# Optimization experiments

Hardware: AMD Instinct MI355X
Metric: run time of the kernel (lower is better)

## Reference

```python
import jax, jax.numpy as jnp
import numpy as np

H = 2048
EPS = 1e-12

def setup_inputs() -> dict:
    key = jax.random.key(0)
    ks = jax.random.split(key, 12)
    B, S = 2, 4096
    scale = 1.0 / np.sqrt(H)
    inp = {
        "hidden_states": jax.random.normal(ks[0], (B, S, H), dtype=jnp.float32),
        "token_type_ids": jax.random.randint(ks[1], (B, S), 0, 2, dtype=jnp.int32),
        "ln_gamma": jnp.ones((H,), jnp.float32),
        "ln_beta": jnp.zeros((H,), jnp.float32),
        "tw1": jax.random.uniform(ks[2], (H, H), jnp.float32, -scale, scale),
        "tb1": jnp.zeros((H,), jnp.float32),
        "tw2": jax.random.uniform(ks[3], (H, H), jnp.float32, -scale, scale),
        "tb2": jnp.zeros((H,), jnp.float32),
        "iw1": jax.random.uniform(ks[4], (H, H), jnp.float32, -scale, scale),
        "ib1": jnp.zeros((H,), jnp.float32),
        "iw2": jax.random.uniform(ks[5], (H, H), jnp.float32, -scale, scale),
        "ib2": jnp.zeros((H,), jnp.float32),
    }
    return inp

def _layernorm(x, g, b):
    mu = jnp.mean(x, axis=-1, keepdims=True)
    var = jnp.mean(jnp.square(x - mu), axis=-1, keepdims=True)
    return (x - mu) * jax.lax.rsqrt(var + EPS) * g + b

def _mlp(x, w1, b1, w2, b2):
    # Linear -> exact GELU -> Linear (torch nn.GELU default is erf-based)
    h = jax.nn.gelu(jnp.einsum('bsh,hk->bsk', x, w1) + b1, approximate=False)
    return jnp.einsum('bsk,kh->bsh', h, w2) + b2

def reference(hidden_states, token_type_ids, ln_gamma, ln_beta,
              tw1, tb1, tw2, tb2, iw1, ib1, iw2, ib2):
    xn = _layernorm(hidden_states, ln_gamma, ln_beta)
    text_mask = (token_type_ids == 0)[..., None]   # [B,S,1]
    image_mask = (token_type_ids == 1)[..., None]
    text_out = _mlp(xn, tw1, tb1, tw2, tb2) * text_mask
    image_out = _mlp(xn, iw1, ib1, iw2, ib2) * image_mask
    # dropout is identity in inference / p=0
    return hidden_states + text_out + image_out
```

## Files before the change

### kernel.cpp

```cpp
#include <hip/hip_runtime.h>
#include <hip/hip_bf16.h>


#define H_DIM 2048
#define FULLROWS 8192
#define TAILROWS 512

typedef __attribute__((ext_vector_type(8))) short s16x8;
typedef __attribute__((ext_vector_type(4))) float f32x4;
typedef __attribute__((ext_vector_type(4))) int   i32x4;

typedef __attribute__((address_space(1))) const unsigned int gu32;
typedef __attribute__((address_space(3))) unsigned int lu32;
typedef __attribute__((address_space(3))) short lds_s;

__device__ __forceinline__ void load_lds16(const void* g, void* l) {
  __builtin_amdgcn_global_load_lds((gu32*)g, (lu32*)l, 16, 0, 0);
}

__device__ __forceinline__ s16x8 asbf(i32x4 v) {
  union { i32x4 i; s16x8 s; } u; u.i = v; return u.s;
}

__global__ __launch_bounds__(256) void partition_kernel(
    const int* __restrict__ tt, int T, int* __restrict__ ctrl,
    int* __restrict__ pos, int* __restrict__ rowid) {
  __shared__ int psum[256];
  const int tid = threadIdx.x;
  const int npt = T >> 8;
  const int base = tid * npt;
  int cnt = 0;
  for (int i = 0; i < npt; ++i) cnt += (tt[base + i] == 0);
  psum[tid] = cnt;
  __syncthreads();
  for (int off = 1; off < 256; off <<= 1) {
    int v = psum[tid];
    int add = (tid >= off) ? psum[tid - off] : 0;
    __syncthreads();
    psum[tid] = v + add;
    __syncthreads();
  }
  const int Mt = psum[255];
  const int Mt_pad = (Mt + 255) & ~255;
  int tpos = psum[tid] - cnt;
  int ipos = base - tpos;
  for (int i = 0; i < npt; ++i) {
    const int tok = base + i;
    int p;
    if (tt[tok] == 0) p = tpos++;
    else              p = Mt_pad + ipos++;
    pos[tok] = p;
    rowid[p] = tok;
  }
  const int Mi = T - Mt;
  const int Mi_pad = (Mi + 255) & ~255;
  for (int g = Mt + tid; g < Mt_pad; g += 256) rowid[g] = -1;
  for (int g = Mt_pad + Mi + tid; g < Mt_pad + Mi_pad; g += 256) rowid[g] = -1;
  for (int g = Mt_pad + Mi_pad + tid; g < FULLROWS + TAILROWS; g += 256)
    rowid[g] = -1;
  if (tid == 0) {
    ctrl[0] = Mt; ctrl[1] = Mt_pad; ctrl[2] = Mi; ctrl[3] = Mi_pad;
    ctrl[4] = Mt_pad + Mi_pad;
  }
}

__global__ __launch_bounds__(256) void pad_zero_kernel(
    const int* __restrict__ ctrl, __hip_bfloat16* __restrict__ XG) {
  const int Mt = ctrl[0], Mt_pad = ctrl[1], Mi = ctrl[2];
  const int n1 = Mt_pad - Mt;
  const int start2 = Mt_pad + Mi;
  const int b = blockIdx.x;
  int row;
  if (b < n1) row = Mt + b;
  else {
    const int b2 = b - n1;
    if (start2 + b2 >= FULLROWS + TAILROWS) return;
    row = start2 + b2;
  }
  const int4 z = {0, 0, 0, 0};
  *(int4*)(XG + (size_t)row * H_DIM + threadIdx.x * 8) = z;
}

__global__ __launch_bounds__(256) void transpose_to_bf16(
    const float* __restrict__ W, __hip_bfloat16* __restrict__ WT) {
  __shared__ float tile[32][33];
  const int bx = blockIdx.x, by = blockIdx.y;
  const int tid = threadIdx.x;
  const int r = tid >> 3, c4 = (tid & 7) * 4;
  const float4 v = *(const float4*)(W + (size_t)(by * 32 + r) * H_DIM + bx * 32 + c4);
  tile[r][c4 + 0] = v.x; tile[r][c4 + 1] = v.y;
  tile[r][c4 + 2] = v.z; tile[r][c4 + 3] = v.w;
  __syncthreads();
  union { ushort u[4]; ushort4 v4; } pk;
#pragma unroll
  for (int j = 0; j < 4; ++j) {
    __hip_bfloat16 h = __float2bfloat16(tile[c4 + j][r]);
    pk.u[j] = *(const ushort*)&h;
  }
  *(ushort4*)(WT + (size_t)(bx * 32 + r) * H_DIM + by * 32 + c4) = pk.v4;
}

__global__ __launch_bounds__(256) void ln_scatter_kernel(
    const float* __restrict__ X, const float* __restrict__ gamma,
    const float* __restrict__ beta, const int* __restrict__ pos,
    __hip_bfloat16* __restrict__ XG) {
  const int t = blockIdx.x, tid = threadIdx.x;
  const float* row = X + (size_t)t * H_DIM;
  float x[8];
  {
    float4 v0 = *(const float4*)(row + tid * 8);
    float4 v1 = *(const float4*)(row + tid * 8 + 4);
    x[0] = v0.x; x[1] = v0.y; x[2] = v0.z; x[3] = v0.w;
    x[4] = v1.x; x[5] = v1.y; x[6] = v1.z; x[7] = v1.w;
  }
  float s = 0.f, q = 0.f;
#pragma unroll
  for (int j = 0; j < 8; ++j) { s += x[j]; q += x[j] * x[j]; }
#pragma unroll
  for (int off = 32; off > 0; off >>= 1) {
    s += __shfl_down(s, off);
    q += __shfl_down(q, off);
  }
  __shared__ float ls[4], lq[4];
  if ((tid & 63) == 0) { ls[tid >> 6] = s; lq[tid >> 6] = q; }
  __syncthreads();
  const float S = ls[0] + ls[1] + ls[2] + ls[3];
  const float Q = lq[0] + lq[1] + lq[2] + lq[3];
  const float mu = S * (1.0f / H_DIM);
  const float var = Q * (1.0f / H_DIM) - mu * mu;
  const float rstd = rsqrtf(var + 1e-12f);
  const int p = pos[t];
  float4 g0 = *(const float4*)(gamma + tid * 8);
  float4 g1 = *(const float4*)(gamma + tid * 8 + 4);
  float4 b0 = *(const float4*)(beta + tid * 8);
  float4 b1 = *(const float4*)(beta + tid * 8 + 4);
  float g[8] = {g0.x, g0.y, g0.z, g0.w, g1.x, g1.y, g1.z, g1.w};
  float b[8] = {b0.x, b0.y, b0.z, b0.w, b1.x, b1.y, b1.z, b1.w};
  union { ushort u[8]; int4 v; } pk;
#pragma unroll
  for (int j = 0; j < 8; ++j) {
    float y = (x[j] - mu) * rstd * g[j] + b[j];
    __hip_bfloat16 h = __float2bfloat16(y);
    pk.u[j] = *(const ushort*)&h;
  }
  *(int4*)(XG + (size_t)p * H_DIM + tid * 8) = pk.v;
}

#define DSRD(dst, addr, OFF) \
  asm volatile("ds_read_b128 %0, %1 offset:" OFF : "=v"(dst) : "v"(addr))
#define PBAR asm volatile("s_barrier" ::: "memory")
#define SB0  __builtin_amdgcn_sched_barrier(0)
#define LGKM0 do { \
  asm volatile("s_waitcnt lgkmcnt(0)" ::: "memory"); SB0; } while (0)
#define VM0 asm volatile("s_waitcnt vmcnt(0)" ::: "memory")

__device__ __forceinline__ float gelu_exact(float z) {
  return 0.5f * z * (1.0f + erff(z * 0.70710678118654752f));
}

template <int EPI>
__global__ __launch_bounds__(512, 2) void gemmk(
    const __hip_bfloat16* __restrict__ A,
    const __hip_bfloat16* __restrict__ WTt, const __hip_bfloat16* __restrict__ WTi,
    const float* __restrict__ bt, const float* __restrict__ bi,
    const int* __restrict__ ctrl, const int* __restrict__ rowid,
    __hip_bfloat16* __restrict__ Hout,
    const float* __restrict__ resid, float* __restrict__ Out,
    float* __restrict__ pp) {
  constexpr int K = H_DIM;
  const int Mt_pad = ctrl[1];

  __shared__ __align__(16) char smem[131072];
  const unsigned sBase = (unsigned)(uintptr_t)(lds_s*)smem;

  const int tid = threadIdx.x;
  const int w = tid >> 6, l = tid & 63;
  const int bid = blockIdx.x;

  const int srow8 = l >> 3;
  const int sg = (l & 7) ^ srow8;
  const int r16 = l & 15;
  const int r4base = (l >> 4) * 4;
  const int hl = (l & 15) >> 1;
  const int gr = (((l & 1) << 2) | (l >> 4)) ^ hl;

  if (bid < 256) {
    constexpr int NT = K / 64;
    const int m0 = (bid >> 3) * 256;
    const int n0 = (bid & 7) * 256;
    const bool is_text = (m0 < Mt_pad);
    const short* Ag = (const short*)A;
    const short* Bg = (const short*)(is_text ? WTt : WTi);
    const float* bias = is_text ? bt : bi;

    const int wm = w >> 2, wn = w & 3;
    const int scol8 = sg * 8;

    auto stageA = [&](int bI, int h, int kk) {
#pragma unroll
      for (int c = 0; c < 2; ++c) {
        const short* src = Ag + (size_t)(m0 + h * 128 + c * 64 + w * 8 + srow8) * K + kk + scol8;
        load_lds16(src, smem + bI * 32768 + h * 16384 + (c * 4096 + w * 512) * 2);
      }
    };
    auto stageB = [&](int bI, int h, int kk) {
#pragma unroll
      for (int c = 0; c < 2; ++c) {
        const short* src = Bg + (size_t)(n0 + h * 128 + c * 64 + w * 8 + srow8) * K + kk + scol8;
        load_lds16(src, smem + 65536 + bI * 32768 + h * 16384 + (c * 4096 + w * 512) * 2);
      }
    };

    int off2[2];
#pragma unroll
    for (int ks = 0; ks < 2; ++ks)
      off2[ks] = r16 * 64 + (((ks * 4 + (l >> 4)) ^ (l & 7)) * 8);

    unsigned ardA[2][2], ardB[2][2];
#pragma unroll
    for (int bI = 0; bI < 2; ++bI)
#pragma unroll
      for (int ks = 0; ks < 2; ++ks) {
        ardA[bI][ks] = sBase + bI * 32768u + (unsigned)(wm * 16384 + off2[ks] * 2);
        ardB[bI][ks] = sBase + 65536u + bI * 32768u +
                       (unsigned)((wn >> 1) * 16384 + ((wn & 1) * 4096 + off2[ks]) * 2);
      }

    i32x4 a[4][2], b[4][2];
    f32x4 acc[8][4];
    const f32x4 zero = {0.f, 0.f, 0.f, 0.f};
#pragma unroll
    for (int i = 0; i < 8; ++i)
#pragma unroll
      for (int j = 0; j < 4; ++j) acc[i][j] = zero;

    auto mfmaQ = [&](int fmBase, int fnBase) {
#pragma unroll
      for (int fm = 0; fm < 4; ++fm)
#pragma unroll
        for (int fn = 0; fn < 2; ++fn)
#pragma unroll
          for (int ks = 0; ks < 2; ++ks)
            acc[fmBase + fm][fnBase + fn] = __builtin_amdgcn_mfma_f32_16x16x32_bf16(
                asbf(a[fm][ks]), asbf(b[fnBase + fn][ks]),
                acc[fmBase + fm][fnBase + fn], 0, 0, 0);
    };

#define TILE(C) do {                                                          \
    DSRD(a[0][0], ardA[C][0], "0");     DSRD(a[0][1], ardA[C][1], "0");       \
    DSRD(a[1][0], ardA[C][0], "2048");  DSRD(a[1][1], ardA[C][1], "2048");    \
    DSRD(a[2][0], ardA[C][0], "4096");  DSRD(a[2][1], ardA[C][1], "4096");    \
    DSRD(a[3][0], ardA[C][0], "6144");  DSRD(a[3][1], ardA[C][1], "6144");    \
    DSRD(b[0][0], ardB[C][0], "0");     DSRD(b[0][1], ardB[C][1], "0");       \
    DSRD(b[1][0], ardB[C][0], "2048");  DSRD(b[1][1], ardB[C][1], "2048");    \
    stageA(C ^ 1, 0, _kA);                                                    \
    PBAR; LGKM0;                                                              \
    __builtin_amdgcn_s_setprio(1); mfmaQ(0, 0); __builtin_amdgcn_s_setprio(0);\
    SB0; PBAR;                                                                \
    DSRD(b[2][0], ardB[C][0], "4096");  DSRD(b[2][1], ardB[C][1], "4096");    \
    DSRD(b[3][0], ardB[C][0], "6144");  DSRD(b[3][1], ardB[C][1], "6144");    \
    stageA(C ^ 1, 1, _kA);                                                    \
    PBAR; LGKM0;                                                              \
    __builtin_amdgcn_s_setprio(1); mfmaQ(0, 2); __builtin_amdgcn_s_setprio(0);\
    SB0; PBAR;                                                                \
    DSRD(a[0][0], ardA[C][0], "8192");  DSRD(a[0][1], ardA[C][1], "8192");    \
    DSRD(a[1][0], ardA[C][0], "10240"); DSRD(a[1][1], ardA[C][1], "10240");   \
    DSRD(a[2][0], ardA[C][0], "12288"); DSRD(a[2][1], ardA[C][1], "12288");   \
    DSRD(a[3][0], ardA[C][0], "14336"); DSRD(a[3][1], ardA[C][1], "14336");   \
    stageB(C, 0, _kB);                                                        \
    PBAR; LGKM0;                                                              \
    __builtin_amdgcn_s_setprio(1); mfmaQ(4, 2); __builtin_amdgcn_s_setprio(0);\
    SB0; PBAR;                                                                \
    stageB(C, 1, _kB);                                                        \
    asm volatile("s_waitcnt vmcnt(4)" ::: "memory");                          \
    PBAR; SB0;                                                                \
    __builtin_amdgcn_s_setprio(1); mfmaQ(4, 0); __builtin_amdgcn_s_setprio(0);\
    SB0; PBAR;                                                                \
  } while (0)

    stageA(0, 0, 0); stageA(0, 1, 0);
    stageB(0, 0, 0); stageB(0, 1, 0);
    stageB(1, 0, 64); stageB(1, 1, 64);
    asm volatile("s_waitcnt vmcnt(4)" ::: "memory");
    PBAR;

    int _kA, _kB;
    for (int t = 0; t < NT; t += 2) {
      _kA = (t + 1 < NT ? t + 1 : NT - 1) * 64;
      _kB = (t + 2 < NT ? t + 2 : NT - 1) * 64;
      TILE(0);
      _kA = (t + 2 < NT ? t + 2 : NT - 1) * 64;
      _kB = (t + 3 < NT ? t + 3 : NT - 1) * 64;
      TILE(1);
    }
#undef TILE
    asm volatile("s_waitcnt vmcnt(0) lgkmcnt(0)" ::: "memory");

    float bb[4];
#pragma unroll
    for (int fn = 0; fn < 4; ++fn) bb[fn] = bias[n0 + wn * 64 + fn * 16 + r16];
    if (EPI == 0) {
#pragma unroll
      for (int fm = 0; fm < 8; ++fm) {
        const int grow = m0 + wm * 128 + fm * 16 + r4base;
#pragma unroll
        for (int fn = 0; fn < 4; ++fn) {
          const int gcol = n0 + wn * 64 + fn * 16 + r16;
          f32x4 v = acc[fm][fn];
#pragma unroll
          for (int i = 0; i < 4; ++i)
            Hout[(size_t)(grow + i) * K + gcol] = __float2bfloat16(gelu_exact(v[i] + bb[fn]));
        }
      }
    } else {
#pragma unroll
      for (int fm = 0; fm < 8; ++fm) {
        const int grow = m0 + wm * 128 + fm * 16 + r4base;
        int rid[4];
#pragma unroll
        for (int i = 0; i < 4; ++i) rid[i] = rowid[grow + i];
#pragma unroll
        for (int fn = 0; fn < 4; ++fn) {
          const int gcol = n0 + wn * 64 + fn * 16 + r16;
          f32x4 v = acc[fm][fn];
#pragma unroll
          for (int i = 0; i < 4; ++i) {
            if (rid[i] >= 0) {
              const size_t o = (size_t)rid[i] * K + gcol;
              Out[o] = resid[o] + v[i] + bb[fn];
            }
          }
        }
      }
    }
  } else {
    const int tb = bid - 256;
    const int kp = tb & 3;
    const int n0 = ((tb >> 2) & 7) * 256;
    const int m0 = FULLROWS + (tb >> 5) * 128;
    const int kk0 = kp * 512;
    const bool is_text = (m0 < Mt_pad);
    const short* Ag = (const short*)A;
    const short* Bg = (const short*)(is_text ? WTt : WTi);

    const int wm = w >> 2, wn = w & 3;
    const int sRowAdj = sg >> 2;
    const int sKAdj = (sg & 3) * 8;

    auto stageA = [&](int bI, int kk) {
      const int mr = w * 8 + srow8;
      const short* src = Ag + (size_t)(m0 + mr * 2 + sRowAdj) * K + kk + sKAdj;
      load_lds16(src, smem + bI * 8192 + w * 1024);
    };
    auto stageB = [&](int bI, int c2, int kk) {
      const int mr = c2 * 64 + w * 8 + srow8;
      const short* src = Bg + (size_t)(n0 + mr * 2 + sRowAdj) * K + kk + sKAdj;
      load_lds16(src, smem + 16384 + bI * 16384 + c2 * 8192 + w * 1024);
    };

    unsigned ardA[2], ardB[2];
#pragma unroll
    for (int bI = 0; bI < 2; ++bI) {
      ardA[bI] = sBase + bI * 8192u + (unsigned)(wm * 4096 + hl * 128 + gr * 16);
      ardB[bI] = sBase + 16384u + bI * 16384u + (unsigned)(wn * 4096 + hl * 128 + gr * 16);
    }

    i32x4 a[4], b[4];
    f32x4 acc[4][4];
    const f32x4 zero = {0.f, 0.f, 0.f, 0.f};
#pragma unroll
    for (int i = 0; i < 4; ++i)
#pragma unroll
      for (int j = 0; j < 4; ++j) acc[i][j] = zero;

#define RD_TILE(C) do {                                                   \
    DSRD(a[0], ardA[C], "0");    DSRD(a[1], ardA[C], "1024");             \
    DSRD(a[2], ardA[C], "2048"); DSRD(a[3], ardA[C], "3072");             \
    DSRD(b[0], ardB[C], "0");    DSRD(b[1], ardB[C], "1024");             \
    DSRD(b[2], ardB[C], "2048"); DSRD(b[3], ardB[C], "3072");             \
  } while (0)

    stageA(0, kk0);
    stageB(0, 0, kk0); stageB(0, 1, kk0);
    VM0;
    PBAR;

    for (int i = 0; i < 16; ++i) {
      const int c = i & 1;
      const int kn = kk0 + (i + 1 < 16 ? i + 1 : 15) * 32;
      stageA(c ^ 1, kn);
      stageB(c ^ 1, 0, kn); stageB(c ^ 1, 1, kn);
      RD_TILE(c);
      LGKM0;
      __builtin_amdgcn_s_setprio(1);
#pragma unroll
      for (int f = 0; f < 4; ++f)
#pragma unroll
        for (int fn = 0; fn < 4; ++fn)
          acc[f][fn] = __builtin_amdgcn_mfma_f32_16x16x32_bf16(
              asbf(a[f]), asbf(b[fn]), acc[f][fn], 0, 0, 0);
      __builtin_amdgcn_s_setprio(0);
      SB0;
      VM0;
      PBAR;
    }
#undef RD_TILE
    asm volatile("s_waitcnt vmcnt(0) lgkmcnt(0)" ::: "memory");

    float* ppk = pp + (size_t)kp * TAILROWS * H_DIM;
    const int mrel = m0 - FULLROWS;
#pragma unroll
    for (int fm = 0; fm < 4; ++fm) {
      const int prow = mrel + wm * 64 + fm * 16 + r4base;
#pragma unroll
      for (int fn = 0; fn < 4; ++fn) {
        const int gcol = n0 + wn * 64 + fn * 16 + r16;
        f32x4 v = acc[fm][fn];
#pragma unroll
        for (int i = 0; i < 4; ++i)
          ppk[(size_t)(prow + i) * H_DIM + gcol] = v[i];
      }
    }
  }
}

template <int EPI>
__global__ __launch_bounds__(256) void combine_kernel(
    const float* __restrict__ pp, const float* __restrict__ bt,
    const float* __restrict__ bi, const int* __restrict__ ctrl,
    const int* __restrict__ rowid, __hip_bfloat16* __restrict__ Hout,
    const float* __restrict__ resid, float* __restrict__ Out) {
  const int u = blockIdx.x * 256 + threadIdx.x;
  const int r = u >> 9;
  const int c = (u & 511) * 4;
  const size_t off = (size_t)r * H_DIM + c;
  float4 s = *(const float4*)(pp + off);
  const float4 s1 = *(const float4*)(pp + (size_t)TAILROWS * H_DIM + off);
  const float4 s2 = *(const float4*)(pp + (size_t)2 * TAILROWS * H_DIM + off);
  const float4 s3 = *(const float4*)(pp + (size_t)3 * TAILROWS * H_DIM + off);
  s.x += s1.x + s2.x + s3.x; s.y += s1.y + s2.y + s3.y;
  s.z += s1.z + s2.z + s3.z; s.w += s1.w + s2.w + s3.w;
  const int grow = FULLROWS + r;
  const float* bias = (grow < ctrl[1]) ? bt : bi;
  const float4 bb = *(const float4*)(bias + c);
  if (EPI == 0) {
    union { ushort u4[4]; ushort4 v4; } pk;
    float z[4] = {s.x + bb.x, s.y + bb.y, s.z + bb.z, s.w + bb.w};
#pragma unroll
    for (int j = 0; j < 4; ++j) {
      __hip_bfloat16 h = __float2bfloat16(0.5f * z[j] * (1.0f + erff(z[j] * 0.70710678118654752f)));
      pk.u4[j] = *(const ushort*)&h;
    }
    *(ushort4*)(Hout + (size_t)grow * H_DIM + c) = pk.v4;
  } else {
    const int rid = rowid[grow];
    if (rid >= 0) {
      const size_t o = (size_t)rid * H_DIM + c;
      const float4 rv = *(const float4*)(resid + o);
      float4 ov;
      ov.x = rv.x + s.x + bb.x; ov.y = rv.y + s.y + bb.y;
      ov.z = rv.z + s.z + bb.z; ov.w = rv.w + s.w + bb.w;
      *(float4*)(Out + o) = ov;
    }
  }
}

extern "C" void kernel_launch(void* const* d_in, const int* in_sizes, int n_in,
                              void* d_out, int out_size, void* d_ws, size_t ws_size,
                              hipStream_t stream) {
  const float* hidden = (const float*)d_in[0];
  const int*   tt     = (const int*)d_in[1];
  const float* gamma  = (const float*)d_in[2];
  const float* beta   = (const float*)d_in[3];
  const float* tw1    = (const float*)d_in[4];
  const float* tb1    = (const float*)d_in[5];
  const float* tw2    = (const float*)d_in[6];
  const float* tb2    = (const float*)d_in[7];
  const float* iw1    = (const float*)d_in[8];
  const float* ib1    = (const float*)d_in[9];
  const float* iw2    = (const float*)d_in[10];
  const float* ib2    = (const float*)d_in[11];
  float* out = (float*)d_out;

  const int T = in_sizes[1];
  const int K = H_DIM;
  const int maxrows = FULLROWS + TAILROWS;

  char* ws = (char*)d_ws;
  int* ctrl  = (int*)(ws);
  int* pos   = (int*)(ws + 4096);
  int* rowid = (int*)(ws + 65536);
  const size_t WOFF = 131072;
  const size_t WSZ = (size_t)K * K * sizeof(__hip_bfloat16);
  __hip_bfloat16* tw1T = (__hip_bfloat16*)(ws + WOFF);
  __hip_bfloat16* tw2T = (__hip_bfloat16*)(ws + WOFF + WSZ);
  __hip_bfloat16* iw1T = (__hip_bfloat16*)(ws + WOFF + 2 * WSZ);
  __hip_bfloat16* iw2T = (__hip_bfloat16*)(ws + WOFF + 3 * WSZ);
  __hip_bfloat16* xg   = (__hip_bfloat16*)(ws + WOFF + 4 * WSZ);
  __hip_bfloat16* hb   = xg + (size_t)maxrows * K;
  float* pp = (float*)(hb + (size_t)maxrows * K);

  partition_kernel<<<1, 256, 0, stream>>>(tt, T, ctrl, pos, rowid);
  pad_zero_kernel<<<512, 256, 0, stream>>>(ctrl, xg);

  dim3 tg(K / 32, K / 32);
  transpose_to_bf16<<<tg, 256, 0, stream>>>(tw1, tw1T);
  transpose_to_bf16<<<tg, 256, 0, stream>>>(tw2, tw2T);
  transpose_to_bf16<<<tg, 256, 0, stream>>>(iw1, iw1T);
  transpose_to_bf16<<<tg, 256, 0, stream>>>(iw2, iw2T);

  ln_scatter_kernel<<<T, 256, 0, stream>>>(hidden, gamma, beta, pos, xg);

  gemmk<0><<<384, 512, 0, stream>>>(xg, tw1T, iw1T, tb1, ib1, ctrl, rowid,
                                    hb, nullptr, nullptr, pp);
  combine_kernel<0><<<1024, 256, 0, stream>>>(pp, tb1, ib1, ctrl, rowid,
                                              hb, nullptr, nullptr);
  gemmk<1><<<384, 512, 0, stream>>>(hb, tw2T, iw2T, tb2, ib2, ctrl, rowid,
                                    nullptr, hidden, out, pp);
  combine_kernel<1><<<1024, 256, 0, stream>>>(pp, tb2, ib2, ctrl, rowid,
                                              nullptr, hidden, out);
}
```

Before: 260.1 us.

## Batch weight transposes into one launch and trim GEMM inner-loop barriers

Merges the four weight transpose-to-bf16 launches into one kernel with a z-grid dimension that picks the weight, which removes three kernel launches. It also restructures the GEMM tile macro so that several workgroup barriers are dropped. The final MFMA quarter now runs before the vmcnt wait and barrier rather than after them. Fewer barriers give more overlap between LDS reads, global-to-LDS staging and MFMA work, but they risk LDS read/write races if a buffer is overwritten before every wave has finished reading it.

```diff
diff --git a/kernel.cpp b/kernel.cpp
--- a/kernel.cpp
+++ b/kernel.cpp
@@ -81,10 +81,15 @@
   *(int4*)(XG + (size_t)row * H_DIM + threadIdx.x * 8) = z;
 }
 
-__global__ __launch_bounds__(256) void transpose_to_bf16(
-    const float* __restrict__ W, __hip_bfloat16* __restrict__ WT) {
+__global__ __launch_bounds__(256) void transpose_to_bf16_x4(
+    const float* __restrict__ W0, const float* __restrict__ W1,
+    const float* __restrict__ W2, const float* __restrict__ W3,
+    __hip_bfloat16* __restrict__ O0, __hip_bfloat16* __restrict__ O1,
+    __hip_bfloat16* __restrict__ O2, __hip_bfloat16* __restrict__ O3) {
   __shared__ float tile[32][33];
-  const int bx = blockIdx.x, by = blockIdx.y;
+  const int bx = blockIdx.x, by = blockIdx.y, bz = blockIdx.z;
+  const float* W = (bz == 0) ? W0 : (bz == 1) ? W1 : (bz == 2) ? W2 : W3;
+  __hip_bfloat16* WT = (bz == 0) ? O0 : (bz == 1) ? O1 : (bz == 2) ? O2 : O3;
   const int tid = threadIdx.x;
   const int r = tid >> 3, c4 = (tid & 7) * 4;
   const float4 v = *(const float4*)(W + (size_t)(by * 32 + r) * H_DIM + bx * 32 + c4);
@@ -247,6 +252,7 @@
     };
 
 #define TILE(C) do {                                                          \
+                                      \
     DSRD(a[0][0], ardA[C][0], "0");     DSRD(a[0][1], ardA[C][1], "0");       \
     DSRD(a[1][0], ardA[C][0], "2048");  DSRD(a[1][1], ardA[C][1], "2048");    \
     DSRD(a[2][0], ardA[C][0], "4096");  DSRD(a[2][1], ardA[C][1], "4096");    \
@@ -256,26 +262,31 @@
     stageA(C ^ 1, 0, _kA);                                                    \
     PBAR; LGKM0;                                                              \
     __builtin_amdgcn_s_setprio(1); mfmaQ(0, 0); __builtin_amdgcn_s_setprio(0);\
-    SB0; PBAR;                                                                \
+    SB0;                                                                      \
+                                             \
     DSRD(b[2][0], ardB[C][0], "4096");  DSRD(b[2][1], ardB[C][1], "4096");    \
     DSRD(b[3][0], ardB[C][0], "6144");  DSRD(b[3][1], ardB[C][1], "6144");    \
     stageA(C ^ 1, 1, _kA);                                                    \
     PBAR; LGKM0;                                                              \
     __builtin_amdgcn_s_setprio(1); mfmaQ(0, 2); __builtin_amdgcn_s_setprio(0);\
-    SB0; PBAR;                                                                \
+    SB0;                                                                      \
+                  \
     DSRD(a[0][0], ardA[C][0], "8192");  DSRD(a[0][1], ardA[C][1], "8192");    \
     DSRD(a[1][0], ardA[C][0], "10240"); DSRD(a[1][1], ardA[C][1], "10240");   \
     DSRD(a[2][0], ardA[C][0], "12288"); DSRD(a[2][1], ardA[C][1], "12288");   \
     DSRD(a[3][0], ardA[C][0], "14336"); DSRD(a[3][1], ardA[C][1], "14336");   \
+    PBAR; LGKM0;                                                              \
     stageB(C, 0, _kB);                                                        \
-    PBAR; LGKM0;                                                              \
+    SB0;                                                                      \
     __builtin_amdgcn_s_setprio(1); mfmaQ(4, 2); __builtin_amdgcn_s_setprio(0);\
-    SB0; PBAR;                                                                \
+    SB0;                                                                      \
+           \
     stageB(C, 1, _kB);                                                        \
+    SB0;                                                                      \
+    __builtin_amdgcn_s_setprio(1); mfmaQ(4, 0); __builtin_amdgcn_s_setprio(0);\
+    SB0;                                                                      \
     asm volatile("s_waitcnt vmcnt(4)" ::: "memory");                          \
-    PBAR; SB0;                                                                \
-    __builtin_amdgcn_s_setprio(1); mfmaQ(4, 0); __builtin_amdgcn_s_setprio(0);\
-    SB0; PBAR;                                                                \
+    PBAR;                                                                     \
   } while (0)
 
     stageA(0, 0, 0); stageA(0, 1, 0);
@@ -503,11 +514,9 @@
   partition_kernel<<<1, 256, 0, stream>>>(tt, T, ctrl, pos, rowid);
   pad_zero_kernel<<<512, 256, 0, stream>>>(ctrl, xg);
 
-  dim3 tg(K / 32, K / 32);
-  transpose_to_bf16<<<tg, 256, 0, stream>>>(tw1, tw1T);
-  transpose_to_bf16<<<tg, 256, 0, stream>>>(tw2, tw2T);
-  transpose_to_bf16<<<tg, 256, 0, stream>>>(iw1, iw1T);
-  transpose_to_bf16<<<tg, 256, 0, stream>>>(iw2, iw2T);
+  dim3 tg(K / 32, K / 32, 4);
+  transpose_to_bf16_x4<<<tg, 256, 0, stream>>>(tw1, tw2, iw1, iw2,
+                                               tw1T, tw2T, iw1T, iw2T);
 
   ln_scatter_kernel<<<T, 256, 0, stream>>>(hidden, gamma, beta, pos, xg);
 
```

Result: faster. 254.6 us (-2.1%).
